# Kernel tuning notes

Hardware: AMD Instinct MI355X
Metric: run time of the kernel (lower is better)

## Reference

```python
import jax, jax.numpy as jnp
import numpy as np

B, IN, OUT = 128, 1024, 1024
BETA, THRESHOLD, RESET = 0.99, 1.0, 0.8
TAU_POS, TAU_NEG = 20.0, 20.0
A_POS, A_NEG = 0.005, 0.005


def setup_inputs() -> dict:
    key = jax.random.key(0)
    k1, k2, k3, k4, k5 = jax.random.split(key, 5)
    in_spikes = (jax.random.uniform(k1, (B, IN)) < 0.1).astype(jnp.float32)
    # nn.Linear default init: U(-1/sqrt(in), 1/sqrt(in))
    bound = 1.0 / np.sqrt(IN)
    W = jax.random.uniform(k2, (OUT, IN), minval=-bound, maxval=bound, dtype=jnp.float32)
    membrane = jax.random.normal(k3, (B, OUT), dtype=jnp.float32) * 0.5
    # trace timers (time since last spike), random in [0, 50)
    delta_pre = jax.random.uniform(k4, (B, IN), dtype=jnp.float32) * 50.0
    delta_fire = jax.random.uniform(k5, (B, OUT), dtype=jnp.float32) * 50.0
    return {"in_spikes": in_spikes, "W": W, "membrane": membrane,
            "delta_pre": delta_pre, "delta_fire": delta_fire}


def reference(in_spikes, W, membrane, delta_pre, delta_fire):
    # dense projection (bias is unused in the original forward)
    weighted = jnp.matmul(in_spikes, W.T)                      # (B, OUT)
    # LIF neuron
    mem = membrane * BETA + weighted
    spike = (mem > THRESHOLD).astype(jnp.float32)
    mem = jnp.where(spike > 0, mem - RESET, mem)
    # trace updates: increment, reset-to-zero where a spike occurred
    dp = jnp.where(in_spikes > 0, 0.0, delta_pre + 1.0)        # (B, IN)
    df = jnp.where(spike > 0, 0.0, delta_fire + 1.0)           # (B, OUT)
    # pairwise timing difference: (B, IN, OUT)
    delta_t = df[:, None, :] - dp[:, :, None]
    potentiation = (delta_t > 0) * (A_POS * jnp.exp(-delta_t / TAU_POS))
    depression = (delta_t < 0) * (A_NEG * jnp.exp(delta_t / TAU_NEG))
    weight_changes = potentiation - depression                 # (B, IN, OUT)
    avg_weight_changes = weight_changes.mean(axis=0).T         # (OUT, IN)
    new_W = W + avg_weight_changes
    return spike, new_W, mem
```

## Files before the change

kernel.cpp:

```cpp
#include <hip/hip_runtime.h>
#include <cstdint>
#include <cmath>

#define Bb   128
#define INN  1024
#define OUTN 1024
#define A_TOT   (0.005f / 128.0f)
#define INV_TAU (1.0f / 20.0f)

__device__ __forceinline__ uint32_t rne_bf16(float f) {
    uint32_t u = __float_as_uint(f);
    return (u + 0x7fffu + ((u >> 16) & 1u)) >> 16;
}

__global__ __launch_bounds__(256) void prep_k(
    const float* __restrict__ W, const float* __restrict__ in_spikes,
    const float* __restrict__ delta_pre,
    float* __restrict__ Wt, uint32_t* __restrict__ IPackB,
    int* __restrict__ gIdx, int* __restrict__ gCount) {
    __shared__ float tile[32][33];
    const int blk = blockIdx.x;
    const int t   = threadIdx.x;

    if ((blk & 3) == 0 && t < 64) {
        const int b = blk >> 2;
        int base = 0;
#pragma unroll
        for (int c = 0; c < 16; c++) {
            float s = in_spikes[(size_t)b * INN + c * 64 + t];
            unsigned long long m = __ballot(s > 0.0f);
            if (s > 0.0f) {
                int pos = base + __popcll(m & ((1ULL << t) - 1ULL));
                gIdx[b * INN + pos] = c * 64 + t;
            }
            base += __popcll(m);
        }
        if (t == 0) gCount[b] = base;
    }

    {
        const int e = blk * 256 + t;
        float sp = in_spikes[e];
        float dp = (sp > 0.0f) ? 0.0f : delta_pre[e] + 1.0f;
        float Iz = expf(-dp * INV_TAU);
        float Iy = A_TOT * expf(dp * INV_TAU);
        IPackB[e] = (rne_bf16(Iz) << 16) | rne_bf16(Iy);
    }

    const int x = t & 31, y = t >> 5;
#pragma unroll
    for (int k = 0; k < 2; k++) {
        int tau = blk * 2 + k;
        int bx = tau & 31, by = tau >> 5;
        __syncthreads();
#pragma unroll
        for (int j = 0; j < 4; j++)
            tile[y + j * 8][x] = W[(size_t)(by * 32 + y + j * 8) * INN + bx * 32 + x];
        __syncthreads();
#pragma unroll
        for (int j = 0; j < 4; j++)
            Wt[(size_t)(bx * 32 + y + j * 8) * OUTN + by * 32 + x] = tile[x][y + j * 8];
    }
}

__global__ __launch_bounds__(256) void spmv_lif_k(
    const float* __restrict__ Wt, const float* __restrict__ membrane,
    const float* __restrict__ delta_fire,
    const int* __restrict__ gIdx, const int* __restrict__ gCount,
    uint32_t* __restrict__ OPackB,
    float* __restrict__ out_spike, float* __restrict__ out_mem) {
    __shared__ int sIdx[INN];
    const int b = blockIdx.x;
    const int z = blockIdx.y;
    const int t = threadIdx.x;
    const int n = gCount[b];
    for (int j = t; j < n; j += 256) sIdx[j] = gIdx[b * INN + j];
    __syncthreads();

    const int o = z * 256 + t;
    float acc = 0.0f;
    int j = 0;
    for (; j + 8 <= n; j += 8) {
        float w0 = Wt[(size_t)sIdx[j + 0] * OUTN + o];
        float w1 = Wt[(size_t)sIdx[j + 1] * OUTN + o];
        float w2 = Wt[(size_t)sIdx[j + 2] * OUTN + o];
        float w3 = Wt[(size_t)sIdx[j + 3] * OUTN + o];
        float w4 = Wt[(size_t)sIdx[j + 4] * OUTN + o];
        float w5 = Wt[(size_t)sIdx[j + 5] * OUTN + o];
        float w6 = Wt[(size_t)sIdx[j + 6] * OUTN + o];
        float w7 = Wt[(size_t)sIdx[j + 7] * OUTN + o];
        acc += ((w0 + w1) + (w2 + w3)) + ((w4 + w5) + (w6 + w7));
    }
    for (; j < n; j++) acc += Wt[(size_t)sIdx[j] * OUTN + o];

    const int n_bo = b * OUTN + o;
    float mem = membrane[n_bo] * 0.99f + acc;
    float s = (mem > 1.0f) ? 1.0f : 0.0f;
    mem = (s > 0.0f) ? mem - 0.8f : mem;
    out_spike[n_bo] = s;
    out_mem[n_bo] = mem;

    float df = (s > 0.0f) ? 0.0f : delta_fire[n_bo] + 1.0f;
    float Oy = expf(-df * INV_TAU);
    float Oz = -A_TOT * expf(df * INV_TAU);
    OPackB[n_bo] = (rne_bf16(Oy) << 16) | rne_bf16(Oz);
}

__global__ __launch_bounds__(256, 2) void stdp_k(const float* __restrict__ W,
                                                 const uint32_t* __restrict__ OPackB,
                                                 const uint32_t* __restrict__ IPackB,
                                                 float* __restrict__ outW) {
    __shared__ uint32_t sO[32][32];
    __shared__ uint32_t sI[32][64];
    const int t  = threadIdx.x;
    const int o0 = blockIdx.x * 32;
    const int i0 = blockIdx.y * 64;
    const int tx = t & 15;
    const int ty = t >> 4;

    float acc[2][4] = {{0.f,0.f,0.f,0.f},{0.f,0.f,0.f,0.f}};

    for (int cb = 0; cb < Bb / 32; cb++) {
        {
            const int row = t >> 3, col = (t & 7) * 4;
            *(uint4*)&sO[row][col] =
                *(const uint4*)&OPackB[(size_t)(cb * 32 + row) * OUTN + o0 + col];
        }
#pragma unroll
        for (int r = 0; r < 2; r++) {
            const int idx = r * 256 + t;
            const int row = idx >> 4, col = (idx & 15) * 4;
            *(uint4*)&sI[row][col] =
                *(const uint4*)&IPackB[(size_t)(cb * 32 + row) * INN + i0 + col];
        }
        __syncthreads();
#pragma unroll
        for (int bb = 0; bb < 32; bb++) {
            uint2 po = *(const uint2*)&sO[bb][2 * ty];
            uint4 pi = *(const uint4*)&sI[bb][4 * tx];
            uint32_t iv[4] = {pi.x, pi.y, pi.z, pi.w};
#pragma unroll
            for (int a = 0; a < 2; a++) {
                const uint32_t o_ = (a == 0) ? po.x : po.y;
#pragma unroll
                for (int c = 0; c < 4; c++) {
                    uint32_t key = min(o_, iv[c]);
                    uint32_t pay = max(o_, iv[c]) << 16;
                    acc[a][c] = fmaf(__uint_as_float(key),
                                     __uint_as_float(pay), acc[a][c]);
                }
            }
        }
        __syncthreads();
    }

#pragma unroll
    for (int a = 0; a < 2; a++) {
        const int o = o0 + 2 * ty + a;
        const size_t off = (size_t)o * INN + i0 + 4 * tx;
        float4 w = *(const float4*)&W[off];
        float4 r = make_float4(w.x + acc[a][0], w.y + acc[a][1],
                               w.z + acc[a][2], w.w + acc[a][3]);
        *(float4*)&outW[off] = r;
    }
}

extern "C" void kernel_launch(void* const* d_in, const int* in_sizes, int n_in,
                              void* d_out, int out_size, void* d_ws, size_t ws_size,
                              hipStream_t stream) {
    const float* in_spikes  = (const float*)d_in[0];
    const float* W          = (const float*)d_in[1];
    const float* membrane   = (const float*)d_in[2];
    const float* delta_pre  = (const float*)d_in[3];
    const float* delta_fire = (const float*)d_in[4];

    float* out_spike = (float*)d_out;
    float* out_W     = out_spike + (size_t)Bb * OUTN;
    float* out_mem   = out_W + (size_t)OUTN * INN;

    float* ws        = (float*)d_ws;
    float* Wt        = ws;
    uint32_t* OPackB = (uint32_t*)(Wt + (size_t)INN * OUTN);
    uint32_t* IPackB = OPackB + (size_t)Bb * OUTN;
    int* gIdx        = (int*)(IPackB + (size_t)Bb * INN);
    int* gCount      = gIdx + (size_t)Bb * INN;

    hipLaunchKernelGGL(prep_k, dim3(512), dim3(256), 0, stream,
                       W, in_spikes, delta_pre, Wt, IPackB, gIdx, gCount);
    hipLaunchKernelGGL(spmv_lif_k, dim3(Bb, 4), dim3(256), 0, stream,
                       Wt, membrane, delta_fire, gIdx, gCount,
                       OPackB, out_spike, out_mem);
    hipLaunchKernelGGL(stdp_k, dim3(OUTN / 32, INN / 64), dim3(256), 0, stream,
                       W, OPackB, IPackB, out_W);
}
```

Before: 101.3 us.

## Split STDP batch reduction across blocks with atomics, copy W in prep

```diff
diff --git a/kernel.cpp b/kernel.cpp
--- a/kernel.cpp
+++ b/kernel.cpp
@@ -17,10 +17,17 @@
     const float* __restrict__ W, const float* __restrict__ in_spikes,
     const float* __restrict__ delta_pre,
     float* __restrict__ Wt, uint32_t* __restrict__ IPackB,
-    int* __restrict__ gIdx, int* __restrict__ gCount) {
+    int* __restrict__ gIdx, int* __restrict__ gCount,
+    float* __restrict__ out_W) {
     __shared__ float tile[32][33];
     const int blk = blockIdx.x;
     const int t   = threadIdx.x;
+
+    {
+        const size_t base = (size_t)blk * 512 + t;
+        ((float4*)out_W)[base]       = ((const float4*)W)[base];
+        ((float4*)out_W)[base + 256] = ((const float4*)W)[base + 256];
+    }
 
     if ((blk & 3) == 0 && t < 64) {
         const int b = blk >> 2;
@@ -106,62 +113,51 @@
     OPackB[n_bo] = (rne_bf16(Oy) << 16) | rne_bf16(Oz);
 }
 
-__global__ __launch_bounds__(256, 2) void stdp_k(const float* __restrict__ W,
-                                                 const uint32_t* __restrict__ OPackB,
-                                                 const uint32_t* __restrict__ IPackB,
-                                                 float* __restrict__ outW) {
-    __shared__ uint32_t sO[32][32];
+__global__ __launch_bounds__(256, 4) void stdp_k(
+    const uint32_t* __restrict__ OPackB, const uint32_t* __restrict__ IPackB,
+    float* __restrict__ out_W) {
+    __shared__ uint32_t sO[32][64];
     __shared__ uint32_t sI[32][64];
-    const int t  = threadIdx.x;
-    const int o0 = blockIdx.x * 32;
-    const int i0 = blockIdx.y * 64;
-    const int tx = t & 15;
-    const int ty = t >> 4;
+    const int t    = threadIdx.x;
+    const int tile = blockIdx.x;
+    const int b0   = blockIdx.y * 32;
+    const int o0 = (tile & 15) * 64, i0 = (tile >> 4) * 64;
+    const int tx = t & 15, ty = t >> 4;
 
-    float acc[2][4] = {{0.f,0.f,0.f,0.f},{0.f,0.f,0.f,0.f}};
+#pragma unroll
+    for (int r = 0; r < 2; r++) {
+        const int idx = r * 256 + t;
+        const int row = idx >> 4, col = (idx & 15) * 4;
+        *(uint4*)&sO[row][col] =
+            *(const uint4*)&OPackB[(size_t)(b0 + row) * OUTN + o0 + col];
+        *(uint4*)&sI[row][col] =
+            *(const uint4*)&IPackB[(size_t)(b0 + row) * INN + i0 + col];
+    }
+    __syncthreads();
 
-    for (int cb = 0; cb < Bb / 32; cb++) {
-        {
-            const int row = t >> 3, col = (t & 7) * 4;
-            *(uint4*)&sO[row][col] =
-                *(const uint4*)&OPackB[(size_t)(cb * 32 + row) * OUTN + o0 + col];
-        }
+    float acc[4][4] = {{0.f}, {0.f}, {0.f}, {0.f}};
 #pragma unroll
-        for (int r = 0; r < 2; r++) {
-            const int idx = r * 256 + t;
-            const int row = idx >> 4, col = (idx & 15) * 4;
-            *(uint4*)&sI[row][col] =
-                *(const uint4*)&IPackB[(size_t)(cb * 32 + row) * INN + i0 + col];
-        }
-        __syncthreads();
+    for (int bb = 0; bb < 32; bb++) {
+        uint4 po = *(const uint4*)&sO[bb][4 * ty];
+        uint4 pi = *(const uint4*)&sI[bb][4 * tx];
+        const uint32_t ov[4] = {po.x, po.y, po.z, po.w};
+        const uint32_t iv[4] = {pi.x, pi.y, pi.z, pi.w};
 #pragma unroll
-        for (int bb = 0; bb < 32; bb++) {
-            uint2 po = *(const uint2*)&sO[bb][2 * ty];
-            uint4 pi = *(const uint4*)&sI[bb][4 * tx];
-            uint32_t iv[4] = {pi.x, pi.y, pi.z, pi.w};
+        for (int a = 0; a < 4; a++)
 #pragma unroll
-            for (int a = 0; a < 2; a++) {
-                const uint32_t o_ = (a == 0) ? po.x : po.y;
-#pragma unroll
-                for (int c = 0; c < 4; c++) {
-                    uint32_t key = min(o_, iv[c]);
-                    uint32_t pay = max(o_, iv[c]) << 16;
-                    acc[a][c] = fmaf(__uint_as_float(key),
-                                     __uint_as_float(pay), acc[a][c]);
-                }
+            for (int c = 0; c < 4; c++) {
+                uint32_t key = min(ov[a], iv[c]);
+                uint32_t pay = max(ov[a], iv[c]) << 16;
+                acc[a][c] = fmaf(__uint_as_float(key),
+                                 __uint_as_float(pay), acc[a][c]);
             }
-        }
-        __syncthreads();
     }
 
 #pragma unroll
-    for (int a = 0; a < 2; a++) {
-        const int o = o0 + 2 * ty + a;
-        const size_t off = (size_t)o * INN + i0 + 4 * tx;
-        float4 w = *(const float4*)&W[off];
-        float4 r = make_float4(w.x + acc[a][0], w.y + acc[a][1],
-                               w.z + acc[a][2], w.w + acc[a][3]);
-        *(float4*)&outW[off] = r;
+    for (int a = 0; a < 4; a++) {
+        float* dst = &out_W[(size_t)(o0 + 4 * ty + a) * INN + i0 + 4 * tx];
+#pragma unroll
+        for (int c = 0; c < 4; c++) atomicAdd(dst + c, acc[a][c]);
     }
 }
 
@@ -186,10 +182,10 @@
     int* gCount      = gIdx + (size_t)Bb * INN;
 
     hipLaunchKernelGGL(prep_k, dim3(512), dim3(256), 0, stream,
-                       W, in_spikes, delta_pre, Wt, IPackB, gIdx, gCount);
+                       W, in_spikes, delta_pre, Wt, IPackB, gIdx, gCount, out_W);
     hipLaunchKernelGGL(spmv_lif_k, dim3(Bb, 4), dim3(256), 0, stream,
                        Wt, membrane, delta_fire, gIdx, gCount,
                        OPackB, out_spike, out_mem);
-    hipLaunchKernelGGL(stdp_k, dim3(OUTN / 32, INN / 64), dim3(256), 0, stream,
-                       W, OPackB, IPackB, out_W);
+    hipLaunchKernelGGL(stdp_k, dim3(256, 4), dim3(256), 0, stream,
+                       OPackB, IPackB, out_W);
 }
```

Measured after the change: 142.4 us. 1.41x slower.
